# Performance work log

Measured on AMD Instinct MI355X. Metric: run time of the kernel, lower is better.

The kernel has to match this reference:

```python
import jax, jax.numpy as jnp
import numpy as np

N_NODES = 100000


def _gcn_conv(x, W, b, src, dst, dinv):
    # PyG GCNConv: h = X @ W; out[i] = sum_{j->i} norm_ji * h[j] (incl. self-loop); + b
    h = x @ W                                   # [N, F_out]
    norm = dinv[src] * dinv[dst]                # [E]
    agg = jax.ops.segment_sum(norm[:, None] * h[src], dst, num_segments=N_NODES)
    agg = agg + (dinv * dinv)[:, None] * h      # self-loop contribution
    return agg + b


def setup_inputs() -> dict:
    key = jax.random.key(0)
    ks = jax.random.split(key, 12)
    N, E, F = N_NODES, 3200000, 128

    def glorot(k, fan_in, fan_out):
        s = float(np.sqrt(6.0 / (fan_in + fan_out)))
        return jax.random.uniform(k, (fan_in, fan_out), jnp.float32, -s, s)

    x = jax.random.normal(ks[0], (N, F), jnp.float32)
    edge_index = jax.random.randint(ks[1], (2, E), 0, N, jnp.int64)
    return {
        "x": x,
        "edge_index": edge_index,
        "W1": glorot(ks[2], F, 64),  "b1": jnp.zeros((64,), jnp.float32),
        "W2": glorot(ks[3], 64, 32), "b2": jnp.zeros((32,), jnp.float32),
        "W3": glorot(ks[4], 32, 16), "b3": jnp.zeros((16,), jnp.float32),
        "Ws02": glorot(ks[5], F, 32),  "bs02": jnp.zeros((32,), jnp.float32),
        "Ws03": glorot(ks[6], F, 16),  "bs03": jnp.zeros((16,), jnp.float32),
        "Ws13": glorot(ks[7], 64, 16), "bs13": jnp.zeros((16,), jnp.float32),
    }


def reference(x, edge_index, W1, b1, W2, b2, W3, b3, Ws02, bs02, Ws03, bs03, Ws13, bs13):
    src, dst = edge_index[0], edge_index[1]
    # symmetric GCN normalization with self-loops: deg[i] = 1 + in-degree(i)
    deg = jax.ops.segment_sum(jnp.ones_like(dst, dtype=x.dtype), dst, num_segments=N_NODES) + 1.0
    dinv = jax.lax.rsqrt(deg)

    # eval-mode: dropout is identity
    x1 = jax.nn.relu(_gcn_conv(x, W1, b1, src, dst, dinv))            # [N, 64]
    x2 = jax.nn.relu(_gcn_conv(x1, W2, b2, src, dst, dinv)) + (x @ Ws02 + bs02)   # [N, 32]
    x3 = (jax.nn.relu(_gcn_conv(x2, W3, b3, src, dst, dinv))
          + (x @ Ws03 + bs03) + (x1 @ Ws13 + bs13))                   # [N, 16]
    return x3
```

## Files before the change

kernel.cpp:

```cpp
#include <hip/hip_runtime.h>

#define NN 100000
#define NB 512
#define NPB 196

__device__ inline unsigned short f2bf(float f) {
    unsigned u = __float_as_uint(f);
    return (unsigned short)((u + 0x7FFFu + ((u >> 16) & 1u)) >> 16);
}
__device__ inline unsigned packbf(float a, float b) {
    return (unsigned)f2bf(a) | ((unsigned)f2bf(b) << 16);
}
__device__ inline float bflo(unsigned u) { return __uint_as_float(u << 16); }
__device__ inline float bfhi(unsigned u) { return __uint_as_float(u & 0xFFFF0000u); }
__device__ inline float4 bf4(uint2 u) {
    return make_float4(bflo(u.x), bfhi(u.x), bflo(u.y), bfhi(u.y));
}

__device__ inline void fp8acc(unsigned u, float4& a) {
    auto lo = __builtin_amdgcn_cvt_pk_f32_fp8((int)u, false);
    auto hi = __builtin_amdgcn_cvt_pk_f32_fp8((int)u, true);
    a.x += lo[0]; a.y += lo[1]; a.z += hi[0]; a.w += hi[1];
}
__device__ inline unsigned char f2fp8(float v) {
    return (unsigned char)(__builtin_amdgcn_cvt_pk_fp8_f32(v, 0.f, 0, false) & 0xFF);
}
__device__ inline unsigned short f2fp8x2(float a, float b) {
    return (unsigned short)(__builtin_amdgcn_cvt_pk_fp8_f32(a, b, 0, false) & 0xFFFF);
}

typedef __attribute__((ext_vector_type(8))) short bf16x8;
typedef __attribute__((ext_vector_type(4))) float f32x4;


__global__ __launch_bounds__(256) void bcount_kernel(const int* __restrict__ dst, int E, int* __restrict__ bcnt) {
    __shared__ int h[NB];
    for (int i = threadIdx.x; i < NB; i += 256) h[i] = 0;
    __syncthreads();
    for (int e = blockIdx.x * 256 + threadIdx.x; e < E; e += gridDim.x * 256)
        atomicAdd(&h[dst[e] / NPB], 1);
    __syncthreads();
    for (int i = threadIdx.x; i < NB; i += 256)
        if (h[i]) atomicAdd(&bcnt[i], h[i]);
}

__global__ __launch_bounds__(512) void bscan_kernel(const int* __restrict__ bcnt, int* __restrict__ bstart,
                                                    int* __restrict__ cursors, int E) {
    __shared__ int sh[NB];
    int t = threadIdx.x;
    int v = bcnt[t];
    sh[t] = v;
    __syncthreads();
    for (int off = 1; off < NB; off <<= 1) {
        int u = (t >= off) ? sh[t - off] : 0;
        __syncthreads();
        sh[t] += u;
        __syncthreads();
    }
    int ex = sh[t] - v;
    bstart[t] = ex;
    cursors[t] = ex;
    if (t == NB - 1) bstart[NB] = E;
}

__global__ __launch_bounds__(256) void multisplit_kernel(const int* __restrict__ src, const int* __restrict__ dst,
                                                         int E, int* __restrict__ cursors,
                                                         unsigned int* __restrict__ packed) {
    __shared__ int cnt[NB];
    __shared__ int base[NB];
    const int CH = 256 * 16;
    int t = threadIdx.x;
    for (long c0 = (long)blockIdx.x * CH; c0 < E; c0 += (long)gridDim.x * CH) {
        for (int i = t; i < NB; i += 256) cnt[i] = 0;
        __syncthreads();
        int s[16], d[16];
        #pragma unroll
        for (int k = 0; k < 16; ++k) {
            long e = c0 + k * 256 + t;
            if (e < E) {
                d[k] = dst[e];
                s[k] = src[e];
                atomicAdd(&cnt[d[k] / NPB], 1);
            } else d[k] = -1;
        }
        __syncthreads();
        for (int i = t; i < NB; i += 256)
            base[i] = cnt[i] ? atomicAdd(&cursors[i], cnt[i]) : 0;
        __syncthreads();
        #pragma unroll
        for (int k = 0; k < 16; ++k) {
            if (d[k] >= 0) {
                int b = d[k] / NPB;
                int ld = d[k] - b * NPB;
                int pos = atomicAdd(&base[b], 1);
                packed[pos] = ((unsigned int)s[k] << 8) | (unsigned int)ld;
            }
        }
        __syncthreads();
    }
}

__global__ __launch_bounds__(256) void bucket_fill_kernel(const unsigned int* __restrict__ packed,
                                                          const int* __restrict__ bstart, int N, int E,
                                                          int* __restrict__ rowptr, int* __restrict__ col,
                                                          float* __restrict__ dinv) {
    int b = blockIdx.x, t = threadIdx.x;
    int e0 = bstart[b], e1 = bstart[b + 1];
    __shared__ int hist[256];
    __shared__ int sh[256];
    __shared__ int cur[256];
    hist[t] = 0;
    __syncthreads();
    for (int e = e0 + t; e < e1; e += 256)
        atomicAdd(&hist[packed[e] & 255u], 1);
    __syncthreads();
    int v = hist[t];
    sh[t] = v;
    __syncthreads();
    for (int off = 1; off < 256; off <<= 1) {
        int u = (t >= off) ? sh[t - off] : 0;
        __syncthreads();
        sh[t] += u;
        __syncthreads();
    }
    int ex = sh[t] - v;
    int node = b * NPB + t;
    if (t < NPB && node < N) {
        rowptr[node] = e0 + ex;
        dinv[node] = rsqrtf(1.0f + (float)v);
    }
    cur[t] = e0 + ex;
    __syncthreads();
    for (int e = e0 + t; e < e1; e += 256) {
        unsigned int p = packed[e];
        int pos = atomicAdd(&cur[p & 255u], 1);
        col[pos] = (int)(p >> 8);
    }
    if (b == 0 && t == 0) rowptr[N] = E;
}


__global__ __launch_bounds__(256) void wpack_kernel(const float* __restrict__ W1, const float* __restrict__ Ws02,
                                                    const float* __restrict__ Ws03, unsigned short* __restrict__ Wpk,
                                                    int* __restrict__ bcnt) {
    if (blockIdx.x < 2) bcnt[blockIdx.x * 256 + threadIdx.x] = 0;
    int i = blockIdx.x * 256 + threadIdx.x;
    if (i >= 112 * 128) return;
    int c = i >> 7, k = i & 127;
    float v;
    if (c < 64)      v = W1[k * 64 + c];
    else if (c < 96) v = Ws02[k * 32 + (c - 64)];
    else             v = Ws03[k * 16 + (c - 96)];
    Wpk[i] = f2bf(v);
}


__global__ __launch_bounds__(256) void mfma3_kernel(const float* __restrict__ X,
        const unsigned short* __restrict__ Wpk, const float* __restrict__ scale,
        const float* __restrict__ bb, const float* __restrict__ bc,
        unsigned char* __restrict__ oa, unsigned short* __restrict__ ob,
        unsigned short* __restrict__ oc, int N) {
    int t = threadIdx.x;
    int wv = t >> 6, l = t & 63;
    int r0 = blockIdx.x * 64 + wv * 16;
    int col = l & 15, g = l >> 4;
    int rowA = r0 + col;
    bool okA = rowA < N;
    const float* xrow = X + (size_t)rowA * 128;

    f32x4 acc[7];
    #pragma unroll
    for (int i = 0; i < 7; ++i) acc[i] = (f32x4){0.f, 0.f, 0.f, 0.f};

    #pragma unroll
    for (int s = 0; s < 4; ++s) {
        int k0 = s * 32 + g * 8;
        float4 lo = okA ? *(const float4*)(xrow + k0)     : make_float4(0.f, 0.f, 0.f, 0.f);
        float4 hi = okA ? *(const float4*)(xrow + k0 + 4) : make_float4(0.f, 0.f, 0.f, 0.f);
        union { bf16x8 v; unsigned u[4]; } A;
        A.u[0] = packbf(lo.x, lo.y);
        A.u[1] = packbf(lo.z, lo.w);
        A.u[2] = packbf(hi.x, hi.y);
        A.u[3] = packbf(hi.z, hi.w);
        #pragma unroll
        for (int ct = 0; ct < 7; ++ct) {
            bf16x8 B = *(const bf16x8*)(Wpk + ((size_t)(ct * 16 + col) * 128 + k0));
            acc[ct] = __builtin_amdgcn_mfma_f32_16x16x32_bf16(A.v, B, acc[ct], 0, 0, 0);
        }
    }

    #pragma unroll
    for (int v = 0; v < 4; ++v) {
        int row = r0 + g * 4 + v;
        if (row < N) {
            float sc = scale[row];
            #pragma unroll
            for (int ct = 0; ct < 4; ++ct)
                oa[(size_t)row * 64 + ct * 16 + col] = f2fp8(acc[ct][v] * sc);
            #pragma unroll
            for (int ct = 4; ct < 6; ++ct) {
                int c2 = (ct - 4) * 16 + col;
                ob[(size_t)row * 32 + c2] = f2bf(acc[ct][v] + bb[c2]);
            }
            oc[(size_t)row * 16 + col] = f2bf(acc[6][v] + bc[col]);
        }
    }
}


template <int K, int C1, int C2>
__global__ __launch_bounds__(256) void gemm2b_kernel(const unsigned short* __restrict__ X,
        const float* __restrict__ Wa, const float* __restrict__ scale,
        const float* __restrict__ Wb, const float* __restrict__ bb,
        unsigned char* __restrict__ oa, unsigned short* __restrict__ ob, int N) {
    constexpr int M1 = C1 / 16, M2 = C2 / 16;
    constexpr int XS = K + 6;
    __shared__ float XL[64 * XS];
    __shared__ float WLa[K * C1];
    __shared__ float WLb[K * C2];
    int t = threadIdx.x;
    int r0 = blockIdx.x * 64;

    for (int i = t; i < K * C1 / 4; i += 256) ((float4*)WLa)[i] = ((const float4*)Wa)[i];
    for (int i = t; i < K * C2 / 4; i += 256) ((float4*)WLb)[i] = ((const float4*)Wb)[i];
    for (int i = t; i < 64 * (K / 4); i += 256) {
        int row = i / (K / 4), g = i % (K / 4);
        uint2 u = make_uint2(0u, 0u);
        if (r0 + row < N) u = ((const uint2*)(X + (size_t)(r0 + row) * K))[g];
        float* p = &XL[row * XS + g * 4];
        *(float2*)p = make_float2(bflo(u.x), bfhi(u.x));
        *(float2*)(p + 2) = make_float2(bflo(u.y), bfhi(u.y));
    }
    __syncthreads();

    int ty = t >> 4, tx = t & 15;
    float acc1[4][M1] = {}, acc2[4][M2] = {};
    const float* xb = &XL[(ty * 4) * XS];
    const float* wba = &WLa[tx * M1];
    const float* wbb = &WLb[tx * M2];
    for (int k = 0; k < K; ++k) {
        float x0 = xb[k], x1 = xb[XS + k], x2 = xb[2 * XS + k], x3 = xb[3 * XS + k];
        float wa[M1], wb2[M2];
        #pragma unroll
        for (int j = 0; j < M1; ++j) wa[j] = wba[k * C1 + j];
        #pragma unroll
        for (int j = 0; j < M2; ++j) wb2[j] = wbb[k * C2 + j];
        #pragma unroll
        for (int j = 0; j < M1; ++j) {
            acc1[0][j] = fmaf(x0, wa[j], acc1[0][j]);
            acc1[1][j] = fmaf(x1, wa[j], acc1[1][j]);
            acc1[2][j] = fmaf(x2, wa[j], acc1[2][j]);
            acc1[3][j] = fmaf(x3, wa[j], acc1[3][j]);
        }
        #pragma unroll
        for (int j = 0; j < M2; ++j) {
            acc2[0][j] = fmaf(x0, wb2[j], acc2[0][j]);
            acc2[1][j] = fmaf(x1, wb2[j], acc2[1][j]);
            acc2[2][j] = fmaf(x2, wb2[j], acc2[2][j]);
            acc2[3][j] = fmaf(x3, wb2[j], acc2[3][j]);
        }
    }

    #pragma unroll
    for (int i = 0; i < 4; ++i) {
        int row = r0 + ty * 4 + i;
        if (row < N) {
            float sc = scale[row];
            *(unsigned short*)(oa + (size_t)row * C1 + tx * 2) = f2fp8x2(acc1[i][0] * sc, acc1[i][1] * sc);
            ob[(size_t)row * C2 + tx] = f2bf(acc2[i][0] + bb[tx]);
        }
    }
}


__global__ __launch_bounds__(256) void gemm_l3_kernel(const unsigned short* __restrict__ X,
        const float* __restrict__ W, const float* __restrict__ scale,
        unsigned char* __restrict__ out, int N) {
    constexpr int K = 32, C = 16, XS = K + 6;
    __shared__ float XL[64 * XS];
    __shared__ float WL[K * C];
    int t = threadIdx.x;
    int r0 = blockIdx.x * 64;

    for (int i = t; i < K * C / 4; i += 256) ((float4*)WL)[i] = ((const float4*)W)[i];
    for (int i = t; i < 64 * (K / 4); i += 256) {
        int row = i / (K / 4), g = i % (K / 4);
        uint2 u = make_uint2(0u, 0u);
        if (r0 + row < N) u = ((const uint2*)(X + (size_t)(r0 + row) * K))[g];
        float* p = &XL[row * XS + g * 4];
        *(float2*)p = make_float2(bflo(u.x), bfhi(u.x));
        *(float2*)(p + 2) = make_float2(bflo(u.y), bfhi(u.y));
    }
    __syncthreads();

    int ty = t >> 4, tx = t & 15;
    float acc[4] = {0.f, 0.f, 0.f, 0.f};
    const float* xb = &XL[(ty * 4) * XS];
    for (int k = 0; k < K; ++k) {
        float wv = WL[k * C + tx];
        acc[0] = fmaf(xb[k], wv, acc[0]);
        acc[1] = fmaf(xb[XS + k], wv, acc[1]);
        acc[2] = fmaf(xb[2 * XS + k], wv, acc[2]);
        acc[3] = fmaf(xb[3 * XS + k], wv, acc[3]);
    }
    #pragma unroll
    for (int i = 0; i < 4; ++i) {
        int row = r0 + ty * 4 + i;
        if (row < N) out[(size_t)row * C + tx] = f2fp8(acc[i] * scale[row]);
    }
}


template <int F, int FPL, bool OBF>
__global__ __launch_bounds__(256) void agg_kernel(const unsigned char* __restrict__ hs,
        const int* __restrict__ rowptr, const int* __restrict__ col,
        const float* __restrict__ dinv, const float* __restrict__ bias,
        const unsigned short* __restrict__ skipA, const unsigned short* __restrict__ skipB,
        void* __restrict__ outv, int N) {
    constexpr int VL = F / FPL;
    constexpr int NPW = 64 / VL;
    constexpr int W = 8;
    constexpr int CR = W / VL;
    int t = threadIdx.x;
    int lane = t & 63, wv = t >> 6;
    int sub = lane / VL, fq = lane % VL;
    int i = (blockIdx.x * 4 + wv) * NPW + sub;
    if (i >= N) return;

    float4 aA0 = make_float4(0.f, 0.f, 0.f, 0.f);
    float4 aA1 = make_float4(0.f, 0.f, 0.f, 0.f);
    float4 aB0 = make_float4(0.f, 0.f, 0.f, 0.f);
    float4 aB1 = make_float4(0.f, 0.f, 0.f, 0.f);

    {
        const unsigned char* hrow = hs + (size_t)i * F + fq * FPL;
        if constexpr (FPL == 8) {
            uint2 u = *(const uint2*)hrow;
            fp8acc(u.x, aA0); fp8acc(u.y, aB0);
        } else {
            fp8acc(*(const unsigned*)hrow, aA0);
        }
    }

    int p0 = rowptr[i], p1 = rowptr[i + 1];
    int p = p0;
    for (; p + W <= p1; p += W) {
        int cw[CR];
        #pragma unroll
        for (int j = 0; j < CR; ++j) cw[j] = col[p + fq + j * VL];
        #pragma unroll
        for (int k = 0; k < W; ++k) {
            int s = __shfl(cw[k / VL], k % VL, VL);
            const unsigned char* sp = hs + (size_t)s * F + fq * FPL;
            if constexpr (FPL == 8) {
                uint2 u = *(const uint2*)sp;
                if (k & 1) { fp8acc(u.x, aA1); fp8acc(u.y, aB1); }
                else       { fp8acc(u.x, aA0); fp8acc(u.y, aB0); }
            } else {
                if (k & 1) fp8acc(*(const unsigned*)sp, aA1);
                else       fp8acc(*(const unsigned*)sp, aA0);
            }
        }
    }
    for (; p < p1; p += VL) {
        int c = (p + fq < p1) ? col[p + fq] : 0;
        int m = min(VL, p1 - p);
        for (int k = 0; k < m; ++k) {
            int s = __shfl(c, k, VL);
            const unsigned char* sp = hs + (size_t)s * F + fq * FPL;
            if constexpr (FPL == 8) {
                uint2 u = *(const uint2*)sp;
                fp8acc(u.x, aA1); fp8acc(u.y, aB1);
            } else {
                fp8acc(*(const unsigned*)sp, aA1);
            }
        }
    }

    float di = dinv[i];
    int fb = fq * FPL;
    float o[FPL];
    o[0] = fmaxf(di * (aA0.x + aA1.x) + bias[fb + 0], 0.f);
    o[1] = fmaxf(di * (aA0.y + aA1.y) + bias[fb + 1], 0.f);
    o[2] = fmaxf(di * (aA0.z + aA1.z) + bias[fb + 2], 0.f);
    o[3] = fmaxf(di * (aA0.w + aA1.w) + bias[fb + 3], 0.f);
    if constexpr (FPL == 8) {
        o[4] = fmaxf(di * (aB0.x + aB1.x) + bias[fb + 4], 0.f);
        o[5] = fmaxf(di * (aB0.y + aB1.y) + bias[fb + 5], 0.f);
        o[6] = fmaxf(di * (aB0.z + aB1.z) + bias[fb + 6], 0.f);
        o[7] = fmaxf(di * (aB0.w + aB1.w) + bias[fb + 7], 0.f);
    }
    if (skipA) {
        const unsigned short* sp = skipA + (size_t)i * F + fb;
        if constexpr (FPL == 8) {
            uint4 sa = *(const uint4*)sp;
            float4 s0 = bf4(make_uint2(sa.x, sa.y)), s1 = bf4(make_uint2(sa.z, sa.w));
            o[0] += s0.x; o[1] += s0.y; o[2] += s0.z; o[3] += s0.w;
            o[4] += s1.x; o[5] += s1.y; o[6] += s1.z; o[7] += s1.w;
        } else {
            float4 s0 = bf4(*(const uint2*)sp);
            o[0] += s0.x; o[1] += s0.y; o[2] += s0.z; o[3] += s0.w;
        }
    }
    if (skipB) {
        const unsigned short* sp = skipB + (size_t)i * F + fb;
        if constexpr (FPL == 8) {
            uint4 sa = *(const uint4*)sp;
            float4 s0 = bf4(make_uint2(sa.x, sa.y)), s1 = bf4(make_uint2(sa.z, sa.w));
            o[0] += s0.x; o[1] += s0.y; o[2] += s0.z; o[3] += s0.w;
            o[4] += s1.x; o[5] += s1.y; o[6] += s1.z; o[7] += s1.w;
        } else {
            float4 s0 = bf4(*(const uint2*)sp);
            o[0] += s0.x; o[1] += s0.y; o[2] += s0.z; o[3] += s0.w;
        }
    }

    if constexpr (OBF) {
        unsigned short* op = (unsigned short*)outv + (size_t)i * F + fb;
        if constexpr (FPL == 8) {
            uint4 w4;
            w4.x = packbf(o[0], o[1]); w4.y = packbf(o[2], o[3]);
            w4.z = packbf(o[4], o[5]); w4.w = packbf(o[6], o[7]);
            *(uint4*)op = w4;
        } else {
            uint2 w2;
            w2.x = packbf(o[0], o[1]); w2.y = packbf(o[2], o[3]);
            *(uint2*)op = w2;
        }
    } else {
        *(float4*)((float*)outv + (size_t)i * F + fb) = make_float4(o[0], o[1], o[2], o[3]);
    }
}


extern "C" void kernel_launch(void* const* d_in, const int* in_sizes, int n_in,
                              void* d_out, int out_size, void* d_ws, size_t ws_size,
                              hipStream_t stream) {
    const int N = NN;
    const float* x   = (const float*)d_in[0];
    const int*   ei  = (const int*)d_in[1];
    const int    E   = in_sizes[1] / 2;
    const int*   src = ei;
    const int*   dst = ei + E;
    const float* W1 = (const float*)d_in[2],  *b1  = (const float*)d_in[3];
    const float* W2 = (const float*)d_in[4],  *b2  = (const float*)d_in[5];
    const float* W3 = (const float*)d_in[6],  *b3  = (const float*)d_in[7];
    const float* Ws02 = (const float*)d_in[8],  *bs02 = (const float*)d_in[9];
    const float* Ws03 = (const float*)d_in[10], *bs03 = (const float*)d_in[11];
    const float* Ws13 = (const float*)d_in[12], *bs13 = (const float*)d_in[13];

    char* w = (char*)d_ws;
    size_t off = 0;
    auto alloc = [&](size_t bytes) -> void* {
        void* p = w + off;
        off += (bytes + 255) & ~(size_t)255;
        return p;
    };
    int*   bcnt     = (int*)alloc((size_t)NB * 4);
    int*   bstart   = (int*)alloc((size_t)(NB + 1) * 4);
    int*   cursors  = (int*)alloc((size_t)NB * 4);
    int*   rowptr   = (int*)alloc(((size_t)N + 1) * 4);
    float* dinv     = (float*)alloc((size_t)N * 4);
    int*   col      = (int*)alloc((size_t)E * 4);
    unsigned short* Wpk = (unsigned short*)alloc((size_t)112 * 128 * 2);
    unsigned char* hs1  = (unsigned char*)alloc((size_t)N * 64 * 2);
    unsigned short* x1  = (unsigned short*)alloc((size_t)N * 64 * 2);
    unsigned short* s02 = (unsigned short*)alloc((size_t)N * 32 * 2);
    unsigned short* s03 = (unsigned short*)alloc((size_t)N * 16 * 2);
    unsigned short* x2  = (unsigned short*)alloc((size_t)N * 32 * 2);
    unsigned int* packed = (unsigned int*)x1;
    unsigned char* hs2 = hs1;
    unsigned short* s13 = (unsigned short*)(hs1 + (size_t)N * 64);
    unsigned char* hs3 = (unsigned char*)s02;

    wpack_kernel<<<(112 * 128 + 255) / 256, 256, 0, stream>>>(W1, Ws02, Ws03, Wpk, bcnt);

    bcount_kernel<<<1024, 256, 0, stream>>>(dst, E, bcnt);
    bscan_kernel<<<1, NB, 0, stream>>>(bcnt, bstart, cursors, E);
    multisplit_kernel<<<(E + 4095) / 4096, 256, 0, stream>>>(src, dst, E, cursors, packed);
    bucket_fill_kernel<<<NB, 256, 0, stream>>>(packed, bstart, N, E, rowptr, col, dinv);

    int gb = (N + 63) / 64;
    mfma3_kernel<<<gb, 256, 0, stream>>>(x, Wpk, dinv, bs02, bs03, hs1, s02, s03, N);
    agg_kernel<64, 8, true><<<(N + 31) / 32, 256, 0, stream>>>(hs1, rowptr, col, dinv, b1, nullptr, nullptr, x1, N);
    gemm2b_kernel<64, 32, 16><<<gb, 256, 0, stream>>>(x1, W2, dinv, Ws13, bs13, hs2, s13, N);
    agg_kernel<32, 8, true><<<(N + 63) / 64, 256, 0, stream>>>(hs2, rowptr, col, dinv, b2, s02, nullptr, x2, N);
    gemm_l3_kernel<<<gb, 256, 0, stream>>>(x2, W3, dinv, hs3, N);
    agg_kernel<16, 4, false><<<(N + 63) / 64, 256, 0, stream>>>(hs3, rowptr, col, dinv, b3, s03, s13, (float*)d_out, N);
}
```

Baseline: 258.8 us.

## Use fewer, larger CSR buckets and LDS-staged multisplit with bigger chunks

Halves the bucket count (256 buckets of 391 nodes) so the CSR bucket fill runs 512-thread blocks over 9-bit local ids. The multisplit kernel now stages 8192 edges per chunk in shared memory instead of holding 16 per thread in registers. This halves the global cursor atomics and the number of blocks, and frees registers. In exchange, each block uses about 42KB of LDS, which may lower occupancy. Larger buckets also mean fewer, longer bucket-fill blocks on a 256-CU-class GPU.

```diff
diff --git a/kernel.cpp b/kernel.cpp
--- a/kernel.cpp
+++ b/kernel.cpp
@@ -1,8 +1,9 @@
 #include <hip/hip_runtime.h>
 
 #define NN 100000
-#define NB 512
-#define NPB 196
+#define NB 256
+#define NPB 391
+#define MSCH 8192
 
 __device__ inline unsigned short f2bf(float f) {
     unsigned u = __float_as_uint(f);
@@ -35,17 +36,16 @@
 
 __global__ __launch_bounds__(256) void bcount_kernel(const int* __restrict__ dst, int E, int* __restrict__ bcnt) {
     __shared__ int h[NB];
-    for (int i = threadIdx.x; i < NB; i += 256) h[i] = 0;
+    if (threadIdx.x < NB) h[threadIdx.x] = 0;
     __syncthreads();
     for (int e = blockIdx.x * 256 + threadIdx.x; e < E; e += gridDim.x * 256)
         atomicAdd(&h[dst[e] / NPB], 1);
     __syncthreads();
-    for (int i = threadIdx.x; i < NB; i += 256)
-        if (h[i]) atomicAdd(&bcnt[i], h[i]);
-}
-
-__global__ __launch_bounds__(512) void bscan_kernel(const int* __restrict__ bcnt, int* __restrict__ bstart,
-                                                    int* __restrict__ cursors, int E) {
+    if (threadIdx.x < NB && h[threadIdx.x]) atomicAdd(&bcnt[threadIdx.x], h[threadIdx.x]);
+}
+
+__global__ __launch_bounds__(NB) void bscan_kernel(const int* __restrict__ bcnt, int* __restrict__ bstart,
+                                                   int* __restrict__ cursors, int E) {
     __shared__ int sh[NB];
     int t = threadIdx.x;
     int v = bcnt[t];
@@ -66,58 +66,54 @@
 __global__ __launch_bounds__(256) void multisplit_kernel(const int* __restrict__ src, const int* __restrict__ dst,
                                                          int E, int* __restrict__ cursors,
                                                          unsigned int* __restrict__ packed) {
+    __shared__ unsigned stage_p[MSCH];
+    __shared__ unsigned char stage_b[MSCH];
     __shared__ int cnt[NB];
     __shared__ int base[NB];
-    const int CH = 256 * 16;
-    int t = threadIdx.x;
-    for (long c0 = (long)blockIdx.x * CH; c0 < E; c0 += (long)gridDim.x * CH) {
-        for (int i = t; i < NB; i += 256) cnt[i] = 0;
-        __syncthreads();
-        int s[16], d[16];
-        #pragma unroll
-        for (int k = 0; k < 16; ++k) {
-            long e = c0 + k * 256 + t;
-            if (e < E) {
-                d[k] = dst[e];
-                s[k] = src[e];
-                atomicAdd(&cnt[d[k] / NPB], 1);
-            } else d[k] = -1;
-        }
-        __syncthreads();
-        for (int i = t; i < NB; i += 256)
-            base[i] = cnt[i] ? atomicAdd(&cursors[i], cnt[i]) : 0;
-        __syncthreads();
-        #pragma unroll
-        for (int k = 0; k < 16; ++k) {
-            if (d[k] >= 0) {
-                int b = d[k] / NPB;
-                int ld = d[k] - b * NPB;
-                int pos = atomicAdd(&base[b], 1);
-                packed[pos] = ((unsigned int)s[k] << 8) | (unsigned int)ld;
-            }
-        }
-        __syncthreads();
-    }
-}
-
-__global__ __launch_bounds__(256) void bucket_fill_kernel(const unsigned int* __restrict__ packed,
+    int t = threadIdx.x;
+    for (long c0 = (long)blockIdx.x * MSCH; c0 < E; c0 += (long)gridDim.x * MSCH) {
+        if (t < NB) cnt[t] = 0;
+        __syncthreads();
+        int nE = (int)min((long)MSCH, E - c0);
+        for (int k = t; k < nE; k += 256) {
+            int d = dst[c0 + k];
+            int s = src[c0 + k];
+            int b = d / NPB;
+            int ld = d - b * NPB;
+            atomicAdd(&cnt[b], 1);
+            stage_p[k] = ((unsigned)s << 9) | (unsigned)ld;
+            stage_b[k] = (unsigned char)b;
+        }
+        __syncthreads();
+        if (t < NB) base[t] = cnt[t] ? atomicAdd(&cursors[t], cnt[t]) : 0;
+        __syncthreads();
+        for (int k = t; k < nE; k += 256) {
+            int b = stage_b[k];
+            int pos = atomicAdd(&base[b], 1);
+            packed[pos] = stage_p[k];
+        }
+        __syncthreads();
+    }
+}
+
+__global__ __launch_bounds__(512) void bucket_fill_kernel(const unsigned int* __restrict__ packed,
                                                           const int* __restrict__ bstart, int N, int E,
                                                           int* __restrict__ rowptr, int* __restrict__ col,
                                                           float* __restrict__ dinv) {
     int b = blockIdx.x, t = threadIdx.x;
     int e0 = bstart[b], e1 = bstart[b + 1];
-    __shared__ int hist[256];
-    __shared__ int sh[256];
-    __shared__ int cur[256];
+    __shared__ int hist[512];
+    __shared__ int sh[512];
+    __shared__ int cur[512];
     hist[t] = 0;
     __syncthreads();
-    for (int e = e0 + t; e < e1; e += 256)
-        atomicAdd(&hist[packed[e] & 255u], 1);
+    for (int e = e0 + t; e < e1; e += 512)
+        atomicAdd(&hist[packed[e] & 511u], 1);
     __syncthreads();
     int v = hist[t];
     sh[t] = v;
     __syncthreads();
-    for (int off = 1; off < 256; off <<= 1) {
+    for (int off = 1; off < 512; off <<= 1) {
         int u = (t >= off) ? sh[t - off] : 0;
         __syncthreads();
         sh[t] += u;
@@ -131,10 +127,10 @@
     }
     cur[t] = e0 + ex;
     __syncthreads();
-    for (int e = e0 + t; e < e1; e += 256) {
+    for (int e = e0 + t; e < e1; e += 512) {
         unsigned int p = packed[e];
-        int pos = atomicAdd(&cur[p & 255u], 1);
-        col[pos] = (int)(p >> 8);
+        int pos = atomicAdd(&cur[p & 511u], 1);
+        col[pos] = (int)(p >> 9);
     }
     if (b == 0 && t == 0) rowptr[N] = E;
 }
@@ -143,7 +139,7 @@
 __global__ __launch_bounds__(256) void wpack_kernel(const float* __restrict__ W1, const float* __restrict__ Ws02,
                                                     const float* __restrict__ Ws03, unsigned short* __restrict__ Wpk,
                                                     int* __restrict__ bcnt) {
-    if (blockIdx.x < 2) bcnt[blockIdx.x * 256 + threadIdx.x] = 0;
+    if (blockIdx.x == 0) bcnt[threadIdx.x] = 0;
     int i = blockIdx.x * 256 + threadIdx.x;
     if (i >= 112 * 128) return;
     int c = i >> 7, k = i & 127;
@@ -477,8 +473,8 @@
 
     bcount_kernel<<<1024, 256, 0, stream>>>(dst, E, bcnt);
     bscan_kernel<<<1, NB, 0, stream>>>(bcnt, bstart, cursors, E);
-    multisplit_kernel<<<(E + 4095) / 4096, 256, 0, stream>>>(src, dst, E, cursors, packed);
-    bucket_fill_kernel<<<NB, 256, 0, stream>>>(packed, bstart, N, E, rowptr, col, dinv);
+    multisplit_kernel<<<(E + MSCH - 1) / MSCH, 256, 0, stream>>>(src, dst, E, cursors, packed);
+    bucket_fill_kernel<<<NB, 512, 0, stream>>>(packed, bstart, N, E, rowptr, col, dinv);
 
     int gb = (N + 63) / 64;
     mfma3_kernel<<<gb, 256, 0, stream>>>(x, Wpk, dinv, bs02, bs03, hs1, s02, s03, N);
```

Result: faster. 243.9 us (-5.8%).
